# Kernel tuning notes

Measured on AMD Instinct MI355X. Metric: run time of the kernel, lower is better.

Reference implementation:

```python
import jax, jax.numpy as jnp
import numpy as np

B, SQ, SKV, D, H = 2, 2048, 2048, 1024, 16
HD = D // H  # 64
ROPE_BASE = 10000.0


def setup_inputs() -> dict:
    key = jax.random.key(0)
    ks = jax.random.split(key, 6)
    s = 1.0 / np.sqrt(D)  # keep activations well-scaled
    return {
        "x_q": jax.random.normal(ks[0], (B, SQ, D), jnp.float32),
        "x_kv": jax.random.normal(ks[1], (B, SKV, D), jnp.float32),
        "wq": jax.random.normal(ks[2], (D, D), jnp.float32) * s,
        "bq": jnp.zeros((D,), jnp.float32),
        "wk": jax.random.normal(ks[3], (D, D), jnp.float32) * s,
        "bk": jnp.zeros((D,), jnp.float32),
        "wv": jax.random.normal(ks[4], (D, D), jnp.float32) * s,
        "bv": jnp.zeros((D,), jnp.float32),
        "wo": jax.random.normal(ks[5], (D, D), jnp.float32) * s,
        "bo": jnp.zeros((D,), jnp.float32),
    }


def _rope_interleaved(x):
    # x: [B, S, H, HD]; sequential positions starting at 0 (GPT-NeoX style)
    s, hd = x.shape[1], x.shape[-1]
    dim = hd // 2
    freqs = jnp.exp(-jnp.arange(dim, dtype=x.dtype) * jnp.log(jnp.asarray(ROPE_BASE, x.dtype)) / dim)
    ang = jnp.arange(s, dtype=x.dtype)[:, None] * freqs[None, :]  # [S, dim]
    cos = jnp.cos(ang)[None, :, None, :]
    sin = jnp.sin(ang)[None, :, None, :]
    xe, xo = x[..., ::2], x[..., 1::2]
    re = xe * cos - xo * sin
    ro = xe * sin + xo * cos
    return jnp.stack([re, ro], axis=-1).reshape(x.shape)


def reference(x_q, x_kv, wq, bq, wk, bk, wv, bv, wo, bo):
    b, sq, _ = x_q.shape
    skv = x_kv.shape[1]
    q = (jnp.einsum("bsd,ed->bse", x_q, wq) + bq).reshape(b, sq, H, HD)
    k = (jnp.einsum("bsd,ed->bse", x_kv, wk) + bk).reshape(b, skv, H, HD)
    v = (jnp.einsum("bsd,ed->bse", x_kv, wv) + bv).reshape(b, skv, H, HD)
    q = _rope_interleaved(q)
    k = _rope_interleaved(k)
    scores = jnp.einsum("bqhd,bkhd->bhqk", q, k) / jnp.sqrt(jnp.asarray(HD, q.dtype))
    attn = jax.nn.softmax(scores, axis=-1)
    ctx = jnp.einsum("bhqk,bkhd->bqhd", attn, v).reshape(b, sq, D)
    return jnp.einsum("bsd,ed->bse", ctx, wo) + bo
```

## Files before the change

### kernel.cpp

```cpp
#include <hip/hip_runtime.h>
#include <cstdint>

typedef __attribute__((ext_vector_type(8))) short bf16x8;
typedef __attribute__((ext_vector_type(4))) float f32x4;
typedef __attribute__((ext_vector_type(4))) unsigned int u32x4;

#define DEV static __device__ __forceinline__

DEV unsigned short f2bf(float f) {
  unsigned int u = __builtin_bit_cast(unsigned int, f);
  u += 0x7FFFu + ((u >> 16) & 1u);
  return (unsigned short)(u >> 16);
}
#if __has_builtin(__builtin_amdgcn_cvt_pk_bf16_f32)
DEV unsigned int pkbf(float a, float b) {
  auto v = __builtin_amdgcn_cvt_pk_bf16_f32(a, b);
  return __builtin_bit_cast(unsigned int, v);
}
#else
DEV unsigned int pkbf(float a, float b) {
  return (unsigned int)f2bf(a) | ((unsigned int)f2bf(b) << 16);
}
#endif
#if __has_builtin(__builtin_amdgcn_exp2f)
#define EXP2(x) __builtin_amdgcn_exp2f(x)
#else
#define EXP2(x) exp2f(x)
#endif
DEV float bfl(unsigned int u) { return __builtin_bit_cast(float, u << 16); }
DEV float bfh(unsigned int u) { return __builtin_bit_cast(float, u & 0xFFFF0000u); }

DEV void async_copy16(const unsigned short* g, unsigned short* l) {
  __builtin_amdgcn_global_load_lds(
      (const __attribute__((address_space(1))) unsigned int*)(uintptr_t)g,
      (__attribute__((address_space(3))) unsigned int*)(uintptr_t)l,
      16, 0, 0);
}

#if __has_builtin(__builtin_amdgcn_permlane32_swap) && \
    __has_builtin(__builtin_amdgcn_permlane16_swap)
DEV void pswap(unsigned a, unsigned b, unsigned& w0, unsigned& w2, int lane) {
  (void)lane;
  auto pq = __builtin_amdgcn_permlane32_swap((int)a, (int)b, false, false);
  auto wz = __builtin_amdgcn_permlane16_swap(pq[0], pq[1], false, false);
  w0 = (unsigned)wz[0];
  w2 = (unsigned)wz[1];
}
#else
DEV void pswap(unsigned a, unsigned b, unsigned& w0, unsigned& w2, int lane) {
  int q = lane >> 4, l = lane & 15;
  int src0 = ((q & 1) << 5) + l;
  int a0 = __shfl((int)a, src0), b0 = __shfl((int)b, src0);
  int a2 = __shfl((int)a, src0 + 16), b2 = __shfl((int)b, src0 + 16);
  w0 = (unsigned)(q < 2 ? a0 : b0);
  w2 = (unsigned)(q < 2 ? a2 : b2);
}
#endif

__global__ __launch_bounds__(256) void cvt8(
    const float* __restrict__ w0, const float* __restrict__ w1,
    const float* __restrict__ w2, const float* __restrict__ w3,
    const float* __restrict__ x0, const float* __restrict__ x1,
    unsigned short* __restrict__ wsb, unsigned short* __restrict__ xb)
{
  int id = blockIdx.x * 256 + threadIdx.x;
  const float* src;
  unsigned short* dp;
  int off;
  if (id < (1 << 20)) {
    int m = id >> 18;
    off = (id & 0x3FFFF) << 2;
    src = m == 0 ? w0 : m == 1 ? w1 : m == 2 ? w2 : w3;
    dp = wsb + (((size_t)m) << 20) + off;
  } else {
    int id2 = id - (1 << 20);
    int m = id2 >> 20;
    off = (id2 & 0xFFFFF) << 2;
    src = m ? x1 : x0;
    dp = xb + (((size_t)m) << 22) + off;
  }
  float4 v = *(const float4*)(src + off);
  uint2 o;
  o.x = pkbf(v.x, v.y);
  o.y = pkbf(v.z, v.w);
  *(uint2*)dp = o;
}

__global__ __launch_bounds__(256) void gemm_qkv_bf(
    const unsigned short* __restrict__ xqb,
    const unsigned short* __restrict__ xkvb,
    const unsigned short* __restrict__ wbase,
    const float* __restrict__ bq, const float* __restrict__ bk,
    const float* __restrict__ bv,
    unsigned short* __restrict__ outq, unsigned short* __restrict__ outk,
    unsigned short* __restrict__ outvT)
{
  constexpr int K = 1024;
  __shared__ unsigned short As[3][128 * 32];
  __shared__ unsigned short Bs[3][128 * 32];
  const int id = blockIdx.x;
  const int sw_id = (id & 7) * 96 + (id >> 3);
  const int z = sw_id >> 8;
  const int r = sw_id & 255;
  const int mBase = (r >> 3) << 7, nBase = (r & 7) << 7;

  const unsigned short* X = (z == 0) ? xqb : xkvb;
  const unsigned short* Wb = wbase + (((size_t)z) << 20);
  const float* bias = (z == 0) ? bq : (z == 1) ? bk : bv;

  const int tid = threadIdx.x;
  const int wave = tid >> 6, lane = tid & 63;
  const int quad = lane >> 4, l16 = lane & 15;
  const int wm = (wave >> 1) << 6, wn = (wave & 1) << 6;

  const int L0 = tid, L1 = 256 + tid;
  const int r0 = L0 >> 2, c0 = ((L0 & 3) ^ (r0 & 3)) << 3;
  const int r1 = L1 >> 2, c1 = ((L1 & 3) ^ (r1 & 3)) << 3;

  f32x4 acc[4][4] = {};

#define QKV_STAGE(kt, bi)                                                     \
  do {                                                                        \
    const int k0_ = (kt) * 32;                                                \
    async_copy16(X + (size_t)(mBase + r0) * K + k0_ + c0, &As[bi][L0 * 8]);   \
    async_copy16(X + (size_t)(mBase + r1) * K + k0_ + c1, &As[bi][L1 * 8]);   \
    async_copy16(Wb + (size_t)(nBase + r0) * K + k0_ + c0, &Bs[bi][L0 * 8]);  \
    async_copy16(Wb + (size_t)(nBase + r1) * K + k0_ + c1, &Bs[bi][L1 * 8]);  \
  } while (0)

  QKV_STAGE(0, 0);
  QKV_STAGE(1, 1);

  const int sw = (quad ^ (l16 & 3)) << 3;
  for (int it = 0; it < 32; ++it) {
    if (it < 31)
      asm volatile("s_waitcnt vmcnt(4)" ::: "memory");
    else
      asm volatile("s_waitcnt vmcnt(0)" ::: "memory");
    __builtin_amdgcn_s_barrier();
    if (it < 30)
      QKV_STAGE(it + 2, (it + 2) % 3);
    const int cur = it % 3;
    bf16x8 af[4], bff[4];
#pragma unroll
    for (int t = 0; t < 4; ++t) {
      af[t]  = *(const bf16x8*)&As[cur][(wm + t * 16 + l16) * 32 + sw];
      bff[t] = *(const bf16x8*)&Bs[cur][(wn + t * 16 + l16) * 32 + sw];
    }
#pragma unroll
    for (int mt = 0; mt < 4; ++mt)
#pragma unroll
      for (int nt = 0; nt < 4; ++nt)
        acc[mt][nt] = __builtin_amdgcn_mfma_f32_16x16x32_bf16(af[mt], bff[nt], acc[mt][nt], 0, 0, 0);
  }
#undef QKV_STAGE

  if (z < 2) {
    unsigned short* out = z ? outk : outq;
    const float qs = z ? 1.0f : 0.18033688011112042f;
    const int sBlk = (mBase & 2047) + wm + quad * 4;
#pragma unroll
    for (int nt = 0; nt < 4; ++nt) {
      int n = nBase + wn + nt * 16 + l16;
      float bv2 = bias[n];
      int h = n >> 6, hd = n & 63;
      int i = hd >> 1;
      int parity = n & 1;
      float f = exp2f(-(float)i * 0.4152410118609203f);
      float sf, cf;
      sincosf(f, &sf, &cf);
#pragma unroll
      for (int mt = 0; mt < 4; ++mt) {
        float ang = (float)(sBlk + mt * 16) * f;
        float s, c;
        sincosf(ang, &s, &c);
#pragma unroll
        for (int j = 0; j < 4; ++j) {
          float v = acc[mt][nt][j] + bv2;
          float pv = __shfl_xor(v, 1);
          float ce = c * qs;
          float se = (parity ? s : -s) * qs;
          float outv = v * ce + pv * se;
          int m = mBase + wm + mt * 16 + quad * 4 + j;
          int b = m >> 11, sv = m & 2047;
          out[(((size_t)(b * 16 + h) * 2048 + sv) << 6) + hd] = f2bf(outv);
          float c2 = c * cf - s * sf;
          s = s * cf + c * sf;
          c = c2;
        }
      }
    }
  } else {
#pragma unroll
    for (int nt = 0; nt < 4; ++nt) {
      int n = nBase + wn + nt * 16 + l16;
      float bv2 = bias[n];
      int h = n >> 6, hd = n & 63;
#pragma unroll
      for (int mt = 0; mt < 4; ++mt) {
        int m0 = mBase + wm + mt * 16 + quad * 4;
        int b = m0 >> 11, s = m0 & 2047;
        uint2 o;
        o.x = pkbf(acc[mt][nt][0] + bv2, acc[mt][nt][1] + bv2);
        o.y = pkbf(acc[mt][nt][2] + bv2, acc[mt][nt][3] + bv2);
        *(uint2*)&outvT[(((size_t)(b * 16 + h) * 64 + hd) << 11) + s] = o;
      }
    }
  }
}

__global__ __launch_bounds__(256) void attn_v8(
    const unsigned short* __restrict__ Qg,
    const unsigned short* __restrict__ Kg,
    const unsigned short* __restrict__ VT,
    unsigned short* __restrict__ Opart,
    float* __restrict__ lbuf)
{
  __shared__ unsigned short Ks[2][64 * 64];
  __shared__ unsigned short Vs[3][64 * 64];
  const int tid = threadIdx.x, wave = tid >> 6, lane = tid & 63;
  const int quad = lane >> 4, l16 = lane & 15;
  const int bh = blockIdx.x & 31;
  const int qt = (blockIdx.x >> 5) & 15;
  const int kvs = blockIdx.x >> 9;
  const int q0 = qt * 128 + wave * 32;
  const unsigned short* Qb = Qg + ((size_t)bh << 17);
  const unsigned short* Kb = Kg + ((size_t)bh << 17);
  const unsigned short* Vb = VT + ((size_t)bh << 17);

  const int L0 = tid, L1 = 256 + tid;
  const int r0 = L0 >> 3, r1 = L1 >> 3;
  const int c0 = ((L0 & 7) ^ (r0 & 7)) << 3;
  const int c1 = ((L1 & 7) ^ (r1 & 7)) << 3;

  bf16x8 qf[2][2];
#pragma unroll
  for (int mq = 0; mq < 2; ++mq)
#pragma unroll
    for (int kd = 0; kd < 2; ++kd)
      qf[mq][kd] = *(const bf16x8*)(Qb + (size_t)(q0 + mq * 16 + l16) * 64 + kd * 32 + quad * 8);

  bf16x8 onesf;
#pragma unroll
  for (int i = 0; i < 8; ++i) onesf[i] = (short)0x3F80;

  f32x4 oacc[4][2] = {};
  f32x4 laccv[2] = {};
  bf16x8 pfp[2][2];

  const int kvbeg = kvs << 10;
  const int swz = l16 & 7;

  async_copy16(Kb + (size_t)(kvbeg + r0) * 64 + c0, &Ks[0][L0 * 8]);
  async_copy16(Kb + (size_t)(kvbeg + r1) * 64 + c1, &Ks[0][L1 * 8]);
  async_copy16(Vb + (size_t)r0 * 2048 + kvbeg + c0, &Vs[0][L0 * 8]);
  async_copy16(Vb + (size_t)r1 * 2048 + kvbeg + c1, &Vs[0][L1 * 8]);
  __syncthreads();

  for (int t = 0; t < 16; ++t) {
    const int kcur = t & 1;
    if (t < 15) {
      const int kv0 = kvbeg + (t + 1) * 64;
      unsigned short* Kn = Ks[kcur ^ 1];
      unsigned short* Vn = Vs[(t + 1) % 3];
      async_copy16(Kb + (size_t)(kv0 + r0) * 64 + c0, &Kn[L0 * 8]);
      async_copy16(Kb + (size_t)(kv0 + r1) * 64 + c1, &Kn[L1 * 8]);
      async_copy16(Vb + (size_t)r0 * 2048 + kv0 + c0, &Vn[L0 * 8]);
      async_copy16(Vb + (size_t)r1 * 2048 + kv0 + c1, &Vn[L1 * 8]);
    }

    if (t > 0) {
      const unsigned short* Vp = Vs[(t - 1) % 3];
      __builtin_amdgcn_s_setprio(1);
#pragma unroll
      for (int ks = 0; ks < 2; ++ks) {
#pragma unroll
        for (int th = 0; th < 4; ++th) {
          bf16x8 vf = *(const bf16x8*)&Vp[(th * 16 + l16) * 64 + (((ks * 4 + quad) ^ swz) << 3)];
#pragma unroll
          for (int mq = 0; mq < 2; ++mq)
            oacc[th][mq] = __builtin_amdgcn_mfma_f32_16x16x32_bf16(vf, pfp[ks][mq], oacc[th][mq], 0, 0, 0);
        }
#pragma unroll
        for (int mq = 0; mq < 2; ++mq)
          laccv[mq] = __builtin_amdgcn_mfma_f32_16x16x32_bf16(onesf, pfp[ks][mq], laccv[mq], 0, 0, 0);
      }
      __builtin_amdgcn_s_setprio(0);
    }

    const unsigned short* Kc = Ks[kcur];
    f32x4 st[4][2] = {};
    __builtin_amdgcn_s_setprio(1);
#pragma unroll
    for (int kd = 0; kd < 2; ++kd)
#pragma unroll
      for (int tk = 0; tk < 4; ++tk) {
        bf16x8 kf = *(const bf16x8*)&Kc[(tk * 16 + l16) * 64 + (((kd * 4 + quad) ^ swz) << 3)];
#pragma unroll
        for (int mq = 0; mq < 2; ++mq)
          st[tk][mq] = __builtin_amdgcn_mfma_f32_16x16x32_bf16(kf, qf[mq][kd], st[tk][mq], 0, 0, 0);
      }
    __builtin_amdgcn_s_setprio(0);

#pragma unroll
    for (int mq = 0; mq < 2; ++mq)
#pragma unroll
      for (int tk = 0; tk < 4; ++tk)
#pragma unroll
        for (int jr = 0; jr < 4; ++jr)
          st[tk][mq][jr] = EXP2(st[tk][mq][jr]);

#pragma unroll
    for (int ks = 0; ks < 2; ++ks)
#pragma unroll
      for (int mq = 0; mq < 2; ++mq) {
        u32x4 pw;
#pragma unroll
        for (int w = 0; w < 2; ++w) {
          unsigned a = pkbf(st[2 * ks][mq][2 * w], st[2 * ks][mq][2 * w + 1]);
          unsigned b = pkbf(st[2 * ks + 1][mq][2 * w], st[2 * ks + 1][mq][2 * w + 1]);
          unsigned w0, w2;
          pswap(a, b, w0, w2, lane);
          pw[w] = w0;
          pw[w + 2] = w2;
        }
        pfp[ks][mq] = __builtin_bit_cast(bf16x8, pw);
      }

    __syncthreads();
  }

  {
    const unsigned short* Vp = Vs[15 % 3];
    __builtin_amdgcn_s_setprio(1);
#pragma unroll
    for (int ks = 0; ks < 2; ++ks) {
#pragma unroll
      for (int th = 0; th < 4; ++th) {
        bf16x8 vf = *(const bf16x8*)&Vp[(th * 16 + l16) * 64 + (((ks * 4 + quad) ^ swz) << 3)];
#pragma unroll
        for (int mq = 0; mq < 2; ++mq)
          oacc[th][mq] = __builtin_amdgcn_mfma_f32_16x16x32_bf16(vf, pfp[ks][mq], oacc[th][mq], 0, 0, 0);
      }
#pragma unroll
      for (int mq = 0; mq < 2; ++mq)
        laccv[mq] = __builtin_amdgcn_mfma_f32_16x16x32_bf16(onesf, pfp[ks][mq], laccv[mq], 0, 0, 0);
    }
    __builtin_amdgcn_s_setprio(0);
  }

  const int b = bh >> 4, h = bh & 15;
  unsigned short* Od = Opart + (((size_t)kvs) << 22);
#pragma unroll
  for (int mq = 0; mq < 2; ++mq) {
    int s = q0 + mq * 16 + l16;
    if (quad == 0)
      lbuf[(kvs * 32 + bh) * 2048 + s] = laccv[mq][0];
#pragma unroll
    for (int th = 0; th < 4; ++th) {
      uint2 o;
      o.x = pkbf(oacc[th][mq][0], oacc[th][mq][1]);
      o.y = pkbf(oacc[th][mq][2], oacc[th][mq][3]);
      *(uint2*)&Od[((size_t)(b * 2048 + s) << 10) + h * 64 + th * 16 + quad * 4] = o;
    }
  }
}

__global__ __launch_bounds__(256) void combine_kernel(
    const unsigned short* __restrict__ Opart, const float* __restrict__ lbuf,
    unsigned short* __restrict__ ctx)
{
  int idx = blockIdx.x * 256 + threadIdx.x;
  int m = idx >> 9;
  int c2 = idx & 511;
  int b = m >> 11, s = m & 2047;
  int h = c2 >> 5;
  int bh = b * 16 + h;
  float la = lbuf[bh * 2048 + s];
  float lb = lbuf[(32 + bh) * 2048 + s];
  float r = 1.0f / (la + lb);
  unsigned int ua = ((const unsigned int*)Opart)[idx];
  unsigned int ub = ((const unsigned int*)Opart)[(1u << 21) + idx];
  float o0 = (bfl(ua) + bfl(ub)) * r;
  float o1 = (bfh(ua) + bfh(ub)) * r;
  ((unsigned int*)ctx)[idx] = pkbf(o0, o1);
}

__global__ __launch_bounds__(256) void gemm_o_bf(
    const unsigned short* __restrict__ X,
    const unsigned short* __restrict__ Wb,
    const float* __restrict__ bias,
    float* __restrict__ out)
{
  constexpr int K = 1024;
  __shared__ unsigned short As[3][64 * 32];
  __shared__ unsigned short Bs[3][128 * 32];
  const int id = blockIdx.x;
  const int sw_id = (id & 7) * 64 + (id >> 3);
  const int mBase = (sw_id >> 3) << 6, nBase = (sw_id & 7) << 7;

  const int tid = threadIdx.x;
  const int wave = tid >> 6, lane = tid & 63;
  const int quad = lane >> 4, l16 = lane & 15;
  const int wm = (wave >> 1) << 5, wn = (wave & 1) << 6;

  const int La = tid, ra = La >> 2, ca = ((La & 3) ^ (ra & 3)) << 3;
  const int Lb1 = 256 + tid, rb1 = Lb1 >> 2, cb1 = ((Lb1 & 3) ^ (rb1 & 3)) << 3;

  f32x4 acc[2][4] = {};

#define O_STAGE(kt, bi)                                                        \
  do {                                                                         \
    const int k0_ = (kt) * 32;                                                 \
    async_copy16(X + (size_t)(mBase + ra) * K + k0_ + ca, &As[bi][La * 8]);    \
    async_copy16(Wb + (size_t)(nBase + ra) * K + k0_ + ca, &Bs[bi][La * 8]);   \
    async_copy16(Wb + (size_t)(nBase + rb1) * K + k0_ + cb1, &Bs[bi][Lb1 * 8]);\
  } while (0)

  O_STAGE(0, 0);
  O_STAGE(1, 1);

  const int sw = (quad ^ (l16 & 3)) << 3;
  for (int it = 0; it < 32; ++it) {
    if (it < 31)
      asm volatile("s_waitcnt vmcnt(3)" ::: "memory");
    else
      asm volatile("s_waitcnt vmcnt(0)" ::: "memory");
    __builtin_amdgcn_s_barrier();
    if (it < 30)
      O_STAGE(it + 2, (it + 2) % 3);
    const int cur = it % 3;
    bf16x8 af[2], bff[4];
#pragma unroll
    for (int t = 0; t < 2; ++t)
      af[t] = *(const bf16x8*)&As[cur][(wm + t * 16 + l16) * 32 + sw];
#pragma unroll
    for (int t = 0; t < 4; ++t)
      bff[t] = *(const bf16x8*)&Bs[cur][(wn + t * 16 + l16) * 32 + sw];
#pragma unroll
    for (int mt = 0; mt < 2; ++mt)
#pragma unroll
      for (int nt = 0; nt < 4; ++nt)
        acc[mt][nt] = __builtin_amdgcn_mfma_f32_16x16x32_bf16(af[mt], bff[nt], acc[mt][nt], 0, 0, 0);
  }
#undef O_STAGE

#pragma unroll
  for (int nt = 0; nt < 4; ++nt) {
    int n = nBase + wn + nt * 16 + l16;
    float bv = bias[n];
#pragma unroll
    for (int mt = 0; mt < 2; ++mt) {
#pragma unroll
      for (int j = 0; j < 4; ++j) {
        int m = mBase + wm + mt * 16 + quad * 4 + j;
        out[((size_t)m << 10) + n] = acc[mt][nt][j] + bv;
      }
    }
  }
}

extern "C" void kernel_launch(void* const* d_in, const int* in_sizes, int n_in,
                              void* d_out, int out_size, void* d_ws, size_t ws_size,
                              hipStream_t stream) {
  const float* x_q  = (const float*)d_in[0];
  const float* x_kv = (const float*)d_in[1];
  const float* wq   = (const float*)d_in[2];
  const float* bq   = (const float*)d_in[3];
  const float* wk   = (const float*)d_in[4];
  const float* bk   = (const float*)d_in[5];
  const float* wv   = (const float*)d_in[6];
  const float* bv   = (const float*)d_in[7];
  const float* wo   = (const float*)d_in[8];
  const float* bo   = (const float*)d_in[9];

  unsigned short* base = (unsigned short*)d_ws;
  unsigned short* ob   = (unsigned short*)d_out;

  unsigned short* wob  = base + (3u << 20);
  unsigned short* k    = base + (4u << 20);
  unsigned short* vT   = base + (8u << 20);
  unsigned short* q    = base + (12u << 20);
  unsigned short* ctx  = q;
  float*          lbuf = (float*)d_ws;
  unsigned short* xqb  = ob;
  unsigned short* xkvb = ob + (4u << 20);
  unsigned short* Opart = ob;
  float* out = (float*)d_out;

  cvt8<<<12288, 256, 0, stream>>>(wq, wk, wv, wo, x_q, x_kv, base, ob);
  gemm_qkv_bf<<<768, 256, 0, stream>>>(xqb, xkvb, base, bq, bk, bv, q, k, vT);
  attn_v8<<<1024, 256, 0, stream>>>(q, k, vT, Opart, lbuf);
  combine_kernel<<<8192, 256, 0, stream>>>(Opart, lbuf, ctx);
  gemm_o_bf<<<512, 256, 0, stream>>>(ctx, wob, bo, out);
}
```

Baseline: 226.1 us.

## Halve QKV GEMM M-tile to 64 and switch to double-buffered loads

The QKV projection GEMM moves from 128x128 tiles with a 3-stage async pipeline to 64x128 tiles with a 2-stage double buffer synchronised by __syncthreads. This doubles the grid to 1536 blocks and cuts LDS use per block, so more blocks fit per CU and the 256 compute units are better covered. In exchange, each block reuses operands less, B tiles are loaded more often in total, and the shallower pipeline with a full barrier each iteration may expose more memory latency.

```diff
diff --git a/kernel.cpp b/kernel.cpp
--- a/kernel.cpp
+++ b/kernel.cpp
@@ -96,13 +96,13 @@
     unsigned short* __restrict__ outvT)
 {
   constexpr int K = 1024;
-  __shared__ unsigned short As[3][128 * 32];
-  __shared__ unsigned short Bs[3][128 * 32];
+  __shared__ unsigned short As[2][64 * 32];
+  __shared__ unsigned short Bs[2][128 * 32];
   const int id = blockIdx.x;
-  const int sw_id = (id & 7) * 96 + (id >> 3);
-  const int z = sw_id >> 8;
-  const int r = sw_id & 255;
-  const int mBase = (r >> 3) << 7, nBase = (r & 7) << 7;
+  const int sw_id = (id & 7) * 192 + (id >> 3);
+  const int z = sw_id >> 9;
+  const int r = sw_id & 511;
+  const int mBase = (r >> 3) << 6, nBase = (r & 7) << 7;
 
   const unsigned short* X = (z == 0) ? xqb : xkvb;
   const unsigned short* Wb = wbase + (((size_t)z) << 20);
@@ -111,49 +111,41 @@
   const int tid = threadIdx.x;
   const int wave = tid >> 6, lane = tid & 63;
   const int quad = lane >> 4, l16 = lane & 15;
-  const int wm = (wave >> 1) << 6, wn = (wave & 1) << 6;
-
-  const int L0 = tid, L1 = 256 + tid;
-  const int r0 = L0 >> 2, c0 = ((L0 & 3) ^ (r0 & 3)) << 3;
-  const int r1 = L1 >> 2, c1 = ((L1 & 3) ^ (r1 & 3)) << 3;
-
-  f32x4 acc[4][4] = {};
-
-#define QKV_STAGE(kt, bi)                                                     \
-  do {                                                                        \
-    const int k0_ = (kt) * 32;                                                \
-    async_copy16(X + (size_t)(mBase + r0) * K + k0_ + c0, &As[bi][L0 * 8]);   \
-    async_copy16(X + (size_t)(mBase + r1) * K + k0_ + c1, &As[bi][L1 * 8]);   \
-    async_copy16(Wb + (size_t)(nBase + r0) * K + k0_ + c0, &Bs[bi][L0 * 8]);  \
-    async_copy16(Wb + (size_t)(nBase + r1) * K + k0_ + c1, &Bs[bi][L1 * 8]);  \
-  } while (0)
-
-  QKV_STAGE(0, 0);
-  QKV_STAGE(1, 1);
+  const int wm = (wave >> 1) << 5, wn = (wave & 1) << 6;
+
+  const int La = tid, ra = La >> 2, ca = ((La & 3) ^ (ra & 3)) << 3;
+  const int Lb1 = 256 + tid, rb1 = Lb1 >> 2, cb1 = ((Lb1 & 3) ^ (rb1 & 3)) << 3;
+
+  f32x4 acc[2][4] = {};
+
+  async_copy16(X + (size_t)(mBase + ra) * K + ca, &As[0][La * 8]);
+  async_copy16(Wb + (size_t)(nBase + ra) * K + ca, &Bs[0][La * 8]);
+  async_copy16(Wb + (size_t)(nBase + rb1) * K + cb1, &Bs[0][Lb1 * 8]);
+  __syncthreads();
 
   const int sw = (quad ^ (l16 & 3)) << 3;
   for (int it = 0; it < 32; ++it) {
-    if (it < 31)
-      asm volatile("s_waitcnt vmcnt(4)" ::: "memory");
-    else
-      asm volatile("s_waitcnt vmcnt(0)" ::: "memory");
-    __builtin_amdgcn_s_barrier();
-    if (it < 30)
-      QKV_STAGE(it + 2, (it + 2) % 3);
-    const int cur = it % 3;
-    bf16x8 af[4], bff[4];
-#pragma unroll
-    for (int t = 0; t < 4; ++t) {
-      af[t]  = *(const bf16x8*)&As[cur][(wm + t * 16 + l16) * 32 + sw];
+    const int cur = it & 1;
+    if (it < 31) {
+      const int k0 = (it + 1) * 32;
+      async_copy16(X + (size_t)(mBase + ra) * K + k0 + ca, &As[cur ^ 1][La * 8]);
+      async_copy16(Wb + (size_t)(nBase + ra) * K + k0 + ca, &Bs[cur ^ 1][La * 8]);
+      async_copy16(Wb + (size_t)(nBase + rb1) * K + k0 + cb1, &Bs[cur ^ 1][Lb1 * 8]);
+    }
+    bf16x8 af[2], bff[4];
+#pragma unroll
+    for (int t = 0; t < 2; ++t)
+      af[t] = *(const bf16x8*)&As[cur][(wm + t * 16 + l16) * 32 + sw];
+#pragma unroll
+    for (int t = 0; t < 4; ++t)
       bff[t] = *(const bf16x8*)&Bs[cur][(wn + t * 16 + l16) * 32 + sw];
-    }
-#pragma unroll
-    for (int mt = 0; mt < 4; ++mt)
+#pragma unroll
+    for (int mt = 0; mt < 2; ++mt)
 #pragma unroll
       for (int nt = 0; nt < 4; ++nt)
         acc[mt][nt] = __builtin_amdgcn_mfma_f32_16x16x32_bf16(af[mt], bff[nt], acc[mt][nt], 0, 0, 0);
-  }
-#undef QKV_STAGE
+    __syncthreads();
+  }
 
   if (z < 2) {
     unsigned short* out = z ? outk : outq;
@@ -170,7 +162,7 @@
       float sf, cf;
       sincosf(f, &sf, &cf);
 #pragma unroll
-      for (int mt = 0; mt < 4; ++mt) {
+      for (int mt = 0; mt < 2; ++mt) {
         float ang = (float)(sBlk + mt * 16) * f;
         float s, c;
         sincosf(ang, &s, &c);
@@ -197,7 +189,7 @@
       float bv2 = bias[n];
       int h = n >> 6, hd = n & 63;
 #pragma unroll
-      for (int mt = 0; mt < 4; ++mt) {
+      for (int mt = 0; mt < 2; ++mt) {
         int m0 = mBase + wm + mt * 16 + quad * 4;
         int b = m0 >> 11, s = m0 & 2047;
         uint2 o;
@@ -489,7 +481,7 @@
   float* out = (float*)d_out;
 
   cvt8<<<12288, 256, 0, stream>>>(wq, wk, wv, wo, x_q, x_kv, base, ob);
-  gemm_qkv_bf<<<768, 256, 0, stream>>>(xqb, xkvb, base, bq, bk, bv, q, k, vT);
+  gemm_qkv_bf<<<1536, 256, 0, stream>>>(xqb, xkvb, base, bq, bk, bv, q, k, vT);
   attn_v8<<<1024, 256, 0, stream>>>(q, k, vT, Opart, lbuf);
   combine_kernel<<<8192, 256, 0, stream>>>(Opart, lbuf, ctx);
   gemm_o_bf<<<512, 256, 0, stream>>>(ctx, wob, bo, out);
```

New measurement: 227.0 us. About the same (+0.4%).
